# Kernel tuning notes

Hardware: AMD Instinct MI355X
Metric: run time of the kernel (lower is better)

The kernel has to match this reference:

```python
import jax, jax.numpy as jnp
import numpy as np

K_WEIGHT = 1.5  # K passed to w() in the original forward
B_EXP = 2.5     # default exponent b in w()


def setup_inputs() -> dict:
    key = jax.random.key(0)
    k1, k2 = jax.random.split(key)
    B, H, D = 4096, 128, 64
    pred = jax.random.normal(k1, (B, H, D), dtype=jnp.float32)
    targ = jax.random.normal(k2, (B, H, D), dtype=jnp.float32)
    return {"pred": pred, "targ": targ}


def reference(pred, targ):
    # pred, targ: [B, H, D]
    B, H, D = pred.shape
    diff = pred - targ                      # loss2
    loss = diff * diff                      # (pred - targ)**2
    # loss3[:, 1:] = diff[:, :-1]; loss3[:, 0] = 0
    loss3 = jnp.concatenate([jnp.zeros_like(diff[:, :1]), diff[:, :-1]], axis=1)
    loss1 = jnp.abs(diff - loss3)           # temporal-difference loss

    # t_i = number of nonzero entries in targ[i, :, 1]
    t = jnp.sum(targ[:, :, 1] != 0, axis=1)              # [B] int
    t_f = t.astype(pred.dtype)
    # w(t, T=H, K=1.5, b=2.5) = 1 + (K-1) * (t/(H-1))**b
    wgt = 1.0 + (K_WEIGHT - 1.0) * (t_f / (H - 1)) ** B_EXP  # [B]

    idx = t - 1
    idx = jnp.where(idx < 0, H - 1, idx)    # mimic torch negative indexing (t=0 -> -1 -> last)

    total = loss + loss1                     # [B, H, D]
    # gather row at index t-1 per sample: [B, D]
    row = jnp.take_along_axis(total, idx[:, None, None], axis=1)[:, 0, :]
    per_sample = wgt * jnp.sum(row, axis=1)  # masked[i, t-1, :] = wgt, summed over H,D
    weighted_loss = jnp.mean(per_sample)
    return weighted_loss
```

## Files before the change

### kernel.cpp

```cpp
#include <hip/hip_runtime.h>
#include <hip/hip_bf16.h>
#include <math.h>


#define H_DIM 128
#define D_DIM 64

__global__ __launch_bounds__(128) void wsl_per_sample_kernel(
    const float* __restrict__ pred,
    const float* __restrict__ targ,
    float* __restrict__ per_sample)
{
    const int i   = blockIdx.x;
    const int tid = threadIdx.x;
    const long long base = (long long)i * (H_DIM * D_DIM);

    float v = targ[base + (long long)tid * D_DIM + 1];
    int flag = (v != 0.0f) ? 1 : 0;

    unsigned long long mask = __ballot(flag);
    __shared__ int wave_cnt[2];
    if ((tid & 63) == 0) wave_cnt[tid >> 6] = __popcll(mask);
    __syncthreads();
    const int t = wave_cnt[0] + wave_cnt[1];

    int idx = t - 1;
    if (idx < 0) idx = H_DIM - 1;

    if (tid < 64) {
        const long long off = base + (long long)idx * D_DIM + tid;
        const float dcur = pred[off] - targ[off];
        float dprev = 0.0f;
        if (idx >= 1) {
            const long long offp = off - D_DIM;
            dprev = pred[offp] - targ[offp];
        }
        float sum = dcur * dcur + fabsf(dcur - dprev);

        #pragma unroll
        for (int sh = 32; sh >= 1; sh >>= 1)
            sum += __shfl_down(sum, sh, 64);

        if (tid == 0) {
            const float tf = (float)t / (float)(H_DIM - 1);
            const float w  = 1.0f + 0.5f * powf(tf, 2.5f);
            per_sample[i] = w * sum;
        }
    }
}

__global__ __launch_bounds__(256) void wsl_finalize_kernel(
    const float* __restrict__ per_sample,
    float* __restrict__ out,
    int B)
{
    __shared__ float s[256];
    const int tid = threadIdx.x;
    float acc = 0.0f;
    for (int j = tid; j < B; j += 256) acc += per_sample[j];
    s[tid] = acc;
    __syncthreads();
    #pragma unroll
    for (int stride = 128; stride >= 1; stride >>= 1) {
        if (tid < stride) s[tid] += s[tid + stride];
        __syncthreads();
    }
    if (tid == 0) out[0] = s[0] / (float)B;
}

extern "C" void kernel_launch(void* const* d_in, const int* in_sizes, int n_in,
                              void* d_out, int out_size, void* d_ws, size_t ws_size,
                              hipStream_t stream)
{
    const float* pred = (const float*)d_in[0];
    const float* targ = (const float*)d_in[1];
    float* out = (float*)d_out;

    const int B = in_sizes[0] / (H_DIM * D_DIM);

    float* per_sample = (float*)d_ws;

    wsl_per_sample_kernel<<<B, 128, 0, stream>>>(pred, targ, per_sample);
    wsl_finalize_kernel<<<1, 256, 0, stream>>>(per_sample, out, B);
}
```

Measured before the change: 22.74 us.

## Process eight samples per block and shrink final reduction to one wave

```diff
diff --git a/kernel.cpp b/kernel.cpp
--- a/kernel.cpp
+++ b/kernel.cpp
@@ -1,71 +1,83 @@
 #include <hip/hip_runtime.h>
-#include <hip/hip_bf16.h>
 #include <math.h>
 
 
 #define H_DIM 128
 #define D_DIM 64
+#define SPB   8
 
-__global__ __launch_bounds__(128) void wsl_per_sample_kernel(
+__global__ __launch_bounds__(256) void wsl_stage1(
     const float* __restrict__ pred,
     const float* __restrict__ targ,
-    float* __restrict__ per_sample)
+    float* __restrict__ block_sums)
 {
-    const int i   = blockIdx.x;
-    const int tid = threadIdx.x;
-    const long long base = (long long)i * (H_DIM * D_DIM);
+    const int tid  = threadIdx.x;
+    const int wave = tid >> 6;
+    const int lane = tid & 63;
+    const int s0   = blockIdx.x * SPB;
 
-    float v = targ[base + (long long)tid * D_DIM + 1];
-    int flag = (v != 0.0f) ? 1 : 0;
+    float colv[4];
+    #pragma unroll
+    for (int k = 0; k < 4; ++k) {
+        const int s = s0 + 2 * k + (tid >> 7);
+        const long long base = (long long)s * (H_DIM * D_DIM);
+        colv[k] = targ[base + (long long)(tid & 127) * D_DIM + 1];
+    }
 
-    unsigned long long mask = __ballot(flag);
-    __shared__ int wave_cnt[2];
-    if ((tid & 63) == 0) wave_cnt[tid >> 6] = __popcll(mask);
+    __shared__ int cnt[4][4];
+    __shared__ float samp[SPB];
+    #pragma unroll
+    for (int k = 0; k < 4; ++k) {
+        const unsigned long long m = __ballot(colv[k] != 0.0f);
+        if (lane == 0) cnt[k][wave] = __popcll(m);
+    }
     __syncthreads();
-    const int t = wave_cnt[0] + wave_cnt[1];
 
-    int idx = t - 1;
-    if (idx < 0) idx = H_DIM - 1;
+    #pragma unroll
+    for (int r = 0; r < 2; ++r) {
+        const int j = wave + 4 * r;
+        const int t = cnt[j >> 1][(j & 1) * 2] + cnt[j >> 1][(j & 1) * 2 + 1];
+        int idx = t - 1;
+        if (idx < 0) idx = H_DIM - 1;
 
-    if (tid < 64) {
-        const long long off = base + (long long)idx * D_DIM + tid;
+        const long long base = (long long)(s0 + j) * (H_DIM * D_DIM);
+        const long long off  = base + (long long)idx * D_DIM + lane;
         const float dcur = pred[off] - targ[off];
         float dprev = 0.0f;
-        if (idx >= 1) {
-            const long long offp = off - D_DIM;
-            dprev = pred[offp] - targ[offp];
-        }
+        if (idx >= 1) dprev = pred[off - D_DIM] - targ[off - D_DIM];
         float sum = dcur * dcur + fabsf(dcur - dprev);
 
         #pragma unroll
         for (int sh = 32; sh >= 1; sh >>= 1)
             sum += __shfl_down(sum, sh, 64);
 
-        if (tid == 0) {
+        if (lane == 0) {
             const float tf = (float)t / (float)(H_DIM - 1);
-            const float w  = 1.0f + 0.5f * powf(tf, 2.5f);
-            per_sample[i] = w * sum;
+            samp[j] = (1.0f + 0.5f * powf(tf, 2.5f)) * sum;
         }
+    }
+    __syncthreads();
+
+    if (tid == 0) {
+        float a = 0.0f;
+        #pragma unroll
+        for (int j = 0; j < SPB; ++j) a += samp[j];
+        block_sums[blockIdx.x] = a;
     }
 }
 
-__global__ __launch_bounds__(256) void wsl_finalize_kernel(
-    const float* __restrict__ per_sample,
+__global__ __launch_bounds__(64) void wsl_stage2(
+    const float* __restrict__ block_sums,
     float* __restrict__ out,
-    int B)
+    int n, float invB)
 {
-    __shared__ float s[256];
-    const int tid = threadIdx.x;
+    const int lane = threadIdx.x;
     float acc = 0.0f;
-    for (int j = tid; j < B; j += 256) acc += per_sample[j];
-    s[tid] = acc;
-    __syncthreads();
+    for (int j = lane; j < n; j += 64) acc += block_sums[j];
     #pragma unroll
-    for (int stride = 128; stride >= 1; stride >>= 1) {
-        if (tid < stride) s[tid] += s[tid + stride];
-        __syncthreads();
-    }
-    if (tid == 0) out[0] = s[0] / (float)B;
+    for (int sh = 32; sh >= 1; sh >>= 1)
+        acc += __shfl_down(acc, sh, 64);
+    if (lane == 0) out[0] = acc * invB;
 }
 
 extern "C" void kernel_launch(void* const* d_in, const int* in_sizes, int n_in,
@@ -77,9 +89,10 @@
     float* out = (float*)d_out;
 
     const int B = in_sizes[0] / (H_DIM * D_DIM);
+    const int nblocks = B / SPB;
 
-    float* per_sample = (float*)d_ws;
+    float* block_sums = (float*)d_ws;
 
-    wsl_per_sample_kernel<<<B, 128, 0, stream>>>(pred, targ, per_sample);
-    wsl_finalize_kernel<<<1, 256, 0, stream>>>(per_sample, out, B);
+    wsl_stage1<<<nblocks, 256, 0, stream>>>(pred, targ, block_sums);
+    wsl_stage2<<<1, 64, 0, stream>>>(block_sums, out, nblocks, 1.0f / (float)B);
 }
```

Measured after the change: 23.45 us. +3.1%, slower.

## Batch two samples per wave and speculatively prefetch last rows

Applied to the files above, without the earlier changes.

```diff
diff --git a/kernel.cpp b/kernel.cpp
--- a/kernel.cpp
+++ b/kernel.cpp
@@ -1,71 +1,96 @@
 #include <hip/hip_runtime.h>
-#include <hip/hip_bf16.h>
 #include <math.h>
 
 
 #define H_DIM 128
 #define D_DIM 64
 
-__global__ __launch_bounds__(128) void wsl_per_sample_kernel(
+__global__ __launch_bounds__(256) void wsl_stage1(
     const float* __restrict__ pred,
     const float* __restrict__ targ,
-    float* __restrict__ per_sample)
+    float* __restrict__ partials,
+    float invB)
 {
-    const int i   = blockIdx.x;
-    const int tid = threadIdx.x;
-    const long long base = (long long)i * (H_DIM * D_DIM);
+    const int wave = threadIdx.x >> 6;
+    const int lane = threadIdx.x & 63;
+    const int sA   = blockIdx.x * 8 + wave * 2;
+    const int sB   = sA + 1;
+    const long long baseA = (long long)sA * (H_DIM * D_DIM);
+    const long long baseB = (long long)sB * (H_DIM * D_DIM);
 
-    float v = targ[base + (long long)tid * D_DIM + 1];
-    int flag = (v != 0.0f) ? 1 : 0;
+    const float cA0 = targ[baseA + (long long)lane * D_DIM + 1];
+    const float cA1 = targ[baseA + (long long)(lane + 64) * D_DIM + 1];
+    const float cB0 = targ[baseB + (long long)lane * D_DIM + 1];
+    const float cB1 = targ[baseB + (long long)(lane + 64) * D_DIM + 1];
+    const float pA_c = pred[baseA + 127 * D_DIM + lane];
+    const float tA_c = targ[baseA + 127 * D_DIM + lane];
+    const float pA_p = pred[baseA + 126 * D_DIM + lane];
+    const float tA_p = targ[baseA + 126 * D_DIM + lane];
+    const float pB_c = pred[baseB + 127 * D_DIM + lane];
+    const float tB_c = targ[baseB + 127 * D_DIM + lane];
+    const float pB_p = pred[baseB + 126 * D_DIM + lane];
+    const float tB_p = targ[baseB + 126 * D_DIM + lane];
 
-    unsigned long long mask = __ballot(flag);
-    __shared__ int wave_cnt[2];
-    if ((tid & 63) == 0) wave_cnt[tid >> 6] = __popcll(mask);
-    __syncthreads();
-    const int t = wave_cnt[0] + wave_cnt[1];
+    const int tA = __popcll(__ballot(cA0 != 0.0f)) + __popcll(__ballot(cA1 != 0.0f));
+    const int tB = __popcll(__ballot(cB0 != 0.0f)) + __popcll(__ballot(cB1 != 0.0f));
 
-    int idx = t - 1;
-    if (idx < 0) idx = H_DIM - 1;
+    float dcurA, dprevA, dcurB, dprevB;
+    if (tA == H_DIM) {
+        dcurA = pA_c - tA_c;  dprevA = pA_p - tA_p;
+    } else {
+        int idx = tA - 1; if (idx < 0) idx = H_DIM - 1;
+        const long long off = baseA + (long long)idx * D_DIM + lane;
+        dcurA = pred[off] - targ[off];
+        dprevA = (idx >= 1) ? (pred[off - D_DIM] - targ[off - D_DIM]) : 0.0f;
+    }
+    if (tB == H_DIM) {
+        dcurB = pB_c - tB_c;  dprevB = pB_p - tB_p;
+    } else {
+        int idx = tB - 1; if (idx < 0) idx = H_DIM - 1;
+        const long long off = baseB + (long long)idx * D_DIM + lane;
+        dcurB = pred[off] - targ[off];
+        dprevB = (idx >= 1) ? (pred[off - D_DIM] - targ[off - D_DIM]) : 0.0f;
+    }
 
-    if (tid < 64) {
-        const long long off = base + (long long)idx * D_DIM + tid;
-        const float dcur = pred[off] - targ[off];
-        float dprev = 0.0f;
-        if (idx >= 1) {
-            const long long offp = off - D_DIM;
-            dprev = pred[offp] - targ[offp];
-        }
-        float sum = dcur * dcur + fabsf(dcur - dprev);
+    float sA_ = dcurA * dcurA + fabsf(dcurA - dprevA);
+    float sB_ = dcurB * dcurB + fabsf(dcurB - dprevB);
 
-        #pragma unroll
-        for (int sh = 32; sh >= 1; sh >>= 1)
-            sum += __shfl_down(sum, sh, 64);
+    #pragma unroll
+    for (int sh = 32; sh >= 1; sh >>= 1) {
+        sA_ += __shfl_down(sA_, sh, 64);
+        sB_ += __shfl_down(sB_, sh, 64);
+    }
 
-        if (tid == 0) {
-            const float tf = (float)t / (float)(H_DIM - 1);
-            const float w  = 1.0f + 0.5f * powf(tf, 2.5f);
-            per_sample[i] = w * sum;
-        }
+    if (lane == 0) {
+        const float fA = (float)tA / (float)(H_DIM - 1);
+        const float fB = (float)tB / (float)(H_DIM - 1);
+        const float wA = 1.0f + 0.5f * powf(fA, 2.5f);
+        const float wB = 1.0f + 0.5f * powf(fB, 2.5f);
+        partials[blockIdx.x * 4 + wave] = (wA * sA_ + wB * sB_) * invB;
     }
 }
 
-__global__ __launch_bounds__(256) void wsl_finalize_kernel(
-    const float* __restrict__ per_sample,
+__global__ __launch_bounds__(256) void wsl_stage2(
+    const float* __restrict__ partials,
     float* __restrict__ out,
-    int B)
+    int n)
 {
     __shared__ float s[256];
     const int tid = threadIdx.x;
     float acc = 0.0f;
-    for (int j = tid; j < B; j += 256) acc += per_sample[j];
+    #pragma unroll
+    for (int k = 0; k < 8; ++k) {
+        const int j = tid + k * 256;
+        if (j < n) acc += partials[j];
+    }
     s[tid] = acc;
     __syncthreads();
     #pragma unroll
-    for (int stride = 128; stride >= 1; stride >>= 1) {
-        if (tid < stride) s[tid] += s[tid + stride];
+    for (int st = 128; st >= 1; st >>= 1) {
+        if (tid < st) s[tid] += s[tid + st];
         __syncthreads();
     }
-    if (tid == 0) out[0] = s[0] / (float)B;
+    if (tid == 0) out[0] = s[0];
 }
 
 extern "C" void kernel_launch(void* const* d_in, const int* in_sizes, int n_in,
@@ -77,9 +102,11 @@
     float* out = (float*)d_out;
 
     const int B = in_sizes[0] / (H_DIM * D_DIM);
+    const int nblocks = B / 8;
+    const int npart = nblocks * 4;
 
-    float* per_sample = (float*)d_ws;
+    float* partials = (float*)d_ws;
 
-    wsl_per_sample_kernel<<<B, 128, 0, stream>>>(pred, targ, per_sample);
-    wsl_finalize_kernel<<<1, 256, 0, stream>>>(per_sample, out, B);
+    wsl_stage1<<<nblocks, 256, 0, stream>>>(pred, targ, partials, 1.0f / (float)B);
+    wsl_stage2<<<1, 256, 0, stream>>>(partials, out, npart);
 }
```

After: 23.00 us. No clear change (+1.1%).
